# Optimization experiments

Hardware: AMD Instinct MI355X
Metric: run time of the kernel (lower is better)

The kernel has to match this reference:

```python
import jax, jax.numpy as jnp
import numpy as np

H = 400      # LSTM hidden units
K = 10       # attention window mixture components (mixtures=30 -> alpha/beta/kappa of size K)
V = 61       # vocab_size
NOUT = 121   # MDN head: 1 eos + 20*(pi, mu1, mu2, sigma1, sigma2, rho)


def setup_inputs():
    key = jax.random.key(0)
    ks = jax.random.split(key, 12)
    B, T, U = 32, 600, 64
    s = 0.05
    d = {}
    d['strokes'] = jax.random.normal(ks[0], (B, T, 3), jnp.float32)
    d['sentence'] = jax.random.uniform(ks[1], (B, U, V), dtype=jnp.float32)
    d['W1'] = jax.random.normal(ks[2], (3 + V, 4 * H), jnp.float32) * s
    d['U1r'] = jax.random.normal(ks[3], (H, 4 * H), jnp.float32) * s
    d['b1'] = jnp.zeros((4 * H,), jnp.float32)
    d['Ww'] = jax.random.normal(ks[4], (H, 3 * K), jnp.float32) * s
    d['bw'] = jnp.zeros((3 * K,), jnp.float32)
    d['W2'] = jax.random.normal(ks[5], (3 + V + H, 4 * H), jnp.float32) * s
    d['U2r'] = jax.random.normal(ks[6], (H, 4 * H), jnp.float32) * s
    d['b2'] = jnp.zeros((4 * H,), jnp.float32)
    d['W3'] = jax.random.normal(ks[7], (3 + V + H, 4 * H), jnp.float32) * s
    d['U3r'] = jax.random.normal(ks[8], (H, 4 * H), jnp.float32) * s
    d['b3'] = jnp.zeros((4 * H,), jnp.float32)
    d['Wm'] = jax.random.normal(ks[9], (3 * H, NOUT), jnp.float32) * s
    d['bm'] = jnp.zeros((NOUT,), jnp.float32)
    return d


def _lstm(x_tbd, W, Ur, b, h0, c0):
    # standard Keras-order (i, f, g, o) LSTM over time-major input [T,B,D]
    def step(carry, xt):
        h, c = carry
        z = xt @ W + h @ Ur + b
        i, f, g, o = jnp.split(z, 4, axis=-1)
        c = jax.nn.sigmoid(f) * c + jax.nn.sigmoid(i) * jnp.tanh(g)
        h = jax.nn.sigmoid(o) * jnp.tanh(c)
        return (h, c), h
    _, hs = jax.lax.scan(step, (h0, c0), x_tbd)
    return hs


def _forward(strokes, sentence, W1, U1r, b1, Ww, bw, W2, U2r, b2, W3, U3r, b3, Wm, bm):
    B, T, _ = strokes.shape
    U = sentence.shape[1]
    u_grid = jnp.arange(U, dtype=strokes.dtype)           # character positions
    x_tb = jnp.transpose(strokes, (1, 0, 2))               # [T,B,3]
    h0 = jnp.zeros((B, H), strokes.dtype)
    w0 = jnp.zeros((B, V), strokes.dtype)
    k0 = jnp.zeros((B, K), strokes.dtype)

    def step1(carry, xt):
        # Graves synthesis windowed LSTM cell: LSTM on [x_t, w_{t-1}],
        # then Gaussian-mixture soft attention over the sentence.
        h, c, w, kappa = carry
        xin = jnp.concatenate([xt, w], axis=-1)            # [B, 3+V]
        z = xin @ W1 + h @ U1r + b1
        i, f, g, o = jnp.split(z, 4, axis=-1)
        c = jax.nn.sigmoid(f) * c + jax.nn.sigmoid(i) * jnp.tanh(g)
        h = jax.nn.sigmoid(o) * jnp.tanh(c)
        p = h @ Ww + bw                                    # [B, 3K]
        alpha = jnp.exp(p[:, :K])
        beta = jnp.exp(p[:, K:2 * K])
        kappa = kappa + jnp.exp(p[:, 2 * K:])
        # phi(u) = sum_k alpha_k exp(-beta_k (kappa_k - u)^2)  -> [B,U]
        phi = jnp.einsum('bk,bku->bu', alpha,
                         jnp.exp(-beta[:, :, None] * (kappa[:, :, None] - u_grid) ** 2))
        w = jnp.einsum('bu,buv->bv', phi, sentence)        # soft window [B,V]
        return (h, c, w, kappa), jnp.concatenate([h, w], axis=-1)

    _, o1 = jax.lax.scan(step1, (h0, h0, w0, k0), x_tb)    # [T,B,H+V]
    lstm1 = o1[:, :, :H]
    win = o1[:, :, H:]
    in2 = jnp.concatenate([x_tb, win, lstm1], axis=-1)     # skip1: [T,B,3+V+H]
    lstm2 = _lstm(in2, W2, U2r, b2, h0, h0)
    in3 = jnp.concatenate([x_tb, win, lstm2], axis=-1)     # skip2
    lstm3 = _lstm(in3, W3, U3r, b3, h0, h0)
    y = jnp.concatenate([lstm1, lstm2, lstm3], axis=-1) @ Wm + bm  # [T,B,121]
    # MDN mixture coefficients
    e = jax.nn.sigmoid(y[..., 0:1])
    pi = jax.nn.softmax(y[..., 1:21], axis=-1)
    mu1 = y[..., 21:41]
    mu2 = y[..., 41:61]
    s1 = jnp.exp(y[..., 61:81])
    s2 = jnp.exp(y[..., 81:101])
    rho = jnp.tanh(y[..., 101:121])
    out = jnp.concatenate([e, pi, mu1, mu2, s1, s2, rho], axis=-1)
    return jnp.transpose(out, (1, 0, 2))                   # [B,T,121]


def reference(strokes, sentence, W1, U1r, b1, Ww, bw, W2, U2r, b2, W3, U3r, b3, Wm, bm):
    return _forward(strokes, sentence, W1, U1r, b1, Ww, bw, W2, U2r, b2, W3, U3r, b3, Wm, bm)
```

## Files before the change

kernel.cpp:

```cpp
#include <hip/hip_runtime.h>
#include <math.h>

#define T 600
#define NBLK 235

#define FL1 256
#define FL2 768
#define FL3 1280
#define FLB 1792
#define SH1 2304
#define SH2 2880
#define SH3 3520

#define OFF_UT1 8192
#define SZ_UT1 (1600*480)
#define OFF_UT2 (OFF_UT1 + SZ_UT1)
#define SZ_UT2 (1600*960)
#define OFF_UT3 (OFF_UT2 + SZ_UT2)
#define OFF_WWT (OFF_UT3 + SZ_UT2)
#define SZ_WWT (30*400)
#define OFF_H1 (OFF_WWT + SZ_WWT)
#define SZ_H (600*32*400)
#define OFF_H2 (OFF_H1 + SZ_H)
#define OFF_H3 (OFF_H2 + SZ_H)
#define OFF_W  (OFF_H3 + SZ_H)
#define SZ_W (600*32*61)

#define LDS_W    0
#define LDS_V    19280
#define LDS_Z    34640
#define LDS_C    35408
#define LDS_TOT  35600

__device__ __forceinline__ float sigm(float x) { return 1.f/(1.f+expf(-x)); }

#define WBAR() do { \
    asm volatile("s_waitcnt lgkmcnt(0)" ::: "memory"); \
    __builtin_amdgcn_sched_barrier(0); \
} while (0)

__global__ void init_ws(unsigned* uws) {
    for (int i = threadIdx.x + blockIdx.x*blockDim.x; i < 8192; i += blockDim.x*gridDim.x)
        uws[i] = 0u;
}

__global__ void build_ut(float* __restrict__ ws,
                         const float* __restrict__ W1, const float* __restrict__ U1r,
                         const float* __restrict__ W2, const float* __restrict__ U2r,
                         const float* __restrict__ W3, const float* __restrict__ U3r,
                         const float* __restrict__ Ww) {
    const long N1 = 1600L*480, N2 = 1600L*960;
    const long total = N1 + 2*N2 + 30L*400;
    for (long i = blockIdx.x*(long)blockDim.x + threadIdx.x; i < total;
         i += (long)gridDim.x*blockDim.x) {
        if (i < N1) {
            long c = i / 480, k = i % 480;
            float v = 0.f;
            if (k < 64) v = W1[k*1600 + c];
            else if (k < 464) v = U1r[(k-64)*1600 + c];
            ws[OFF_UT1 + c*480 + k] = v;
        } else if (i < N1 + N2) {
            long ii = i - N1; long c = ii/960, k = ii%960;
            float v = 0.f;
            if (k < 464) v = W2[k*1600 + c];
            else if (k >= 480 && k < 880) v = U2r[(k-480)*1600 + c];
            ws[OFF_UT2 + c*960 + k] = v;
        } else if (i < N1 + 2*N2) {
            long ii = i - N1 - N2; long c = ii/960, k = ii%960;
            float v = 0.f;
            if (k < 464) v = W3[k*1600 + c];
            else if (k >= 480 && k < 880) v = U3r[(k-480)*1600 + c];
            ws[OFF_UT3 + c*960 + k] = v;
        } else {
            long ii = i - N1 - 2*N2; long n = ii/400, k = ii%400;
            ws[OFF_WWT + n*400 + k] = Ww[k*30 + n];
        }
    }
}

__device__ __forceinline__ unsigned ld_cohere(const unsigned* p) {
    unsigned v;
    asm volatile("global_load_dword %0, %1, off sc0 sc1\n\t"
                 "s_waitcnt vmcnt(0)"
                 : "=v"(v) : "v"(p) : "memory");
    return v;
}
__device__ __forceinline__ void st_wt(float* p, float v) {
    asm volatile("global_store_dword %0, %1, off sc0 sc1\n\t"
                 "s_waitcnt vmcnt(0)"
                 :: "v"(p), "v"(v) : "memory");
}
__device__ __forceinline__ void publish(unsigned* flags, unsigned v) {
    #pragma unroll
    for (int r = 0; r < 8; ++r)
        asm volatile("global_store_dword %0, %1, off sc0 sc1"
                     :: "v"(flags + r*64), "v"(v) : "memory");
    asm volatile("s_waitcnt vmcnt(0)" ::: "memory");
}
__device__ __forceinline__ void wait_flag(const unsigned* p, unsigned tgt) {
    int it = 0;
    while (ld_cohere(p) < tgt) {
        if (it > 64) __builtin_amdgcn_s_sleep(2);
        ++it;
    }
}
__device__ __forceinline__ void arrive2(unsigned* shard, unsigned gsize,
                                        unsigned* master, unsigned n,
                                        unsigned* flags, unsigned ep1) {
    unsigned old = __hip_atomic_fetch_add(shard, 1u, __ATOMIC_RELAXED,
                                          __HIP_MEMORY_SCOPE_AGENT);
    if (old + 1u == gsize * ep1) {
        unsigned o2 = __hip_atomic_fetch_add(master, gsize, __ATOMIC_RELAXED,
                                             __HIP_MEMORY_SCOPE_AGENT);
        if (o2 + gsize == n * ep1) publish(flags, ep1);
    }
}
__device__ __forceinline__ void arrive1(unsigned* master, unsigned n,
                                        unsigned* flags, unsigned ep1) {
    unsigned old = __hip_atomic_fetch_add(master, 1u, __ATOMIC_RELAXED,
                                          __HIP_MEMORY_SCOPE_AGENT);
    if (old + 1u == n * ep1) publish(flags, ep1);
}

template<int NQ, int KCN, int K4S, int LO, int HI>
__device__ __forceinline__ void gemm_pass(const float4* __restrict__ w4,
                                          const float4* __restrict__ v4,
                                          int lc0, int kc, int bq, int kofs4,
                                          float acc[8][4]) {
    #pragma unroll
    for (int q = 0; q < NQ; ++q) {
        int kfv = q*KCN + kc;
        if (kfv >= LO && kfv < HI) {
            int xv = kfv ^ ((kfv >> 3) & 7);
            int kfw = kofs4 + kfv;
            int xw = kfw ^ ((kfw >> 3) & 7);
            float4 va[8];
            #pragma unroll
            for (int i = 0; i < 8; ++i) va[i] = v4[(bq*8+i)*120 + xv];
            #pragma unroll
            for (int j = 0; j < 4; ++j) {
                float4 u = w4[(lc0+j)*K4S + xw];
                #pragma unroll
                for (int i = 0; i < 8; ++i)
                    acc[i][j] += va[i].x*u.x + va[i].y*u.y + va[i].z*u.z + va[i].w*u.w;
            }
        }
    }
}

__launch_bounds__(512)
__global__ void hw_main(float* __restrict__ ws,
                        const float* __restrict__ strokes, const float* __restrict__ sentence,
                        const float* __restrict__ b1, const float* __restrict__ b2,
                        const float* __restrict__ b3, const float* __restrict__ bw) {
    extern __shared__ float S[];
    const int tid = threadIdx.x;
    const int bid = blockIdx.x;
    unsigned* uws = (unsigned*)ws;
    unsigned* root1 = uws + 0;
    unsigned* root2 = uws + 64;
    unsigned* root3 = uws + 128;
    unsigned* rootB = uws + 192;
    const int rep = (bid & 7) * 64;
    const unsigned* fl1r = uws + FL1 + rep;
    const unsigned* fl2r = uws + FL2 + rep;
    const unsigned* flBr = uws + FLB + rep;

    int role, unit0 = 0, nu = 0, L = 0, b0a = 0;
    const float* utp = nullptr; const float* biasp = nullptr; float* hout = nullptr;
    if (bid < 67)       { role = 0; L = bid;      unit0 = L*6; nu = (bid==66)?4:6; utp = ws+OFF_UT1; biasp = b1; hout = ws+OFF_H1; }
    else if (bid < 147) { role = 1; L = bid-67;   unit0 = L*5; nu = 5;             utp = ws+OFF_UT2; biasp = b2; hout = ws+OFF_H2; }
    else if (bid < 227) { role = 2; L = bid-147;  unit0 = L*5; nu = 5;             utp = ws+OFF_UT3; biasp = b3; hout = ws+OFF_H3; }
    else                { role = 3; b0a = (bid-227)*4; }

    if (role <= 2) {
        const int NC = 4*nu;
        const int KCN = (role == 0) ? 20 : 24;
        const int K4S = (role == 0) ? 121 : 241;
        const int K4TOT = (role == 0) ? 120 : 240;
        const int uts = (role == 0) ? 480 : 960;
        float4* w4 = (float4*)S;
        float4* v4 = (float4*)(S + LDS_V);
        float*  vf = S + LDS_V;
        float*  z_lds = S + LDS_Z;
        float*  c_lds = S + LDS_C;

        for (int idx = tid; idx < NC*K4TOT; idx += 512) {
            int colL = idx / K4TOT, kf = idx % K4TOT;
            int gcol = (colL/nu)*400 + unit0 + (colL%nu);
            float4 val = *(const float4*)(utp + (size_t)gcol*uts + kf*4);
            w4[colL*K4S + (kf ^ ((kf>>3)&7))] = val;
        }
        for (int i = tid; i < 192; i += 512) c_lds[i] = 0.f;

        const int tile = tid / KCN, kc = tid % KCN;
        const int bq = tile / nu, cq = tile % nu;
        const bool act = (tile < 4*nu);
        float bias0 = 0.f, bias1 = 0.f;
        if (tid < 32*NC)       { int lc = tid % NC;        bias0 = biasp[(lc/nu)*400 + unit0 + (lc%nu)]; }
        if (tid + 512 < 32*NC) { int lc = (tid+512) % NC;  bias1 = biasp[(lc/nu)*400 + unit0 + (lc%nu)]; }
        const unsigned nrole = (role == 0) ? 67u : 80u;
        unsigned* mymaster = (role == 0) ? root1 : ((role == 1) ? root2 : root3);
        unsigned* myfl     = uws + ((role == 0) ? FL1 : ((role == 1) ? FL2 : FL3));
        const unsigned* myflr = uws + ((role == 0) ? FL1 : ((role == 1) ? FL2 : FL3)) + rep;
        unsigned* myshard;
        {
            int shbase = (role == 0) ? SH1 : ((role == 1) ? SH2 : SH3);
            myshard = uws + shbase + (L >> 3) * 64;
        }
        const unsigned gsize = (unsigned)(((int)nrole - (L >> 3)*8 < 8) ? ((int)nrole - (L >> 3)*8) : 8);
        __syncthreads();

        for (int t = 0; t < T; ++t) {
            float acc[8][4];
            #pragma unroll
            for (int i = 0; i < 8; ++i)
                #pragma unroll
                for (int j = 0; j < 4; ++j) acc[i][j] = 0.f;

            if (role == 0) {
                if (tid == 0 && t > 0) wait_flag(myflr, (unsigned)t);
                __syncthreads();
                const float* hsrc = (t > 0) ? (ws + OFF_H1 + (size_t)(t-1)*12800) : nullptr;
                for (int idx = tid; idx < 32*104; idx += 512) {
                    int b = idx/104, kf = 16 + idx%104;
                    float4 val = {0.f,0.f,0.f,0.f};
                    if (kf < 116 && hsrc) val = *(const float4*)(hsrc + b*400 + (kf*4 - 64));
                    v4[b*120 + (kf ^ ((kf>>3)&7))] = val;
                }
                __syncthreads();
                if (act) gemm_pass<6,20,121,16,116>(w4, v4, cq*4, kc, bq, 0, acc);
                if (tid == 0 && t > 0) wait_flag(flBr, (unsigned)t);
                __syncthreads();
                const float* wsrc = (t > 0) ? (ws + OFF_W + (size_t)(t-1)*1952) : nullptr;
                {
                    int b = tid / 16, kf = tid % 16;
                    if (b < 32) {
                        float4 val;
                        if (kf == 0) {
                            const float* xp = strokes + ((size_t)b*600 + t)*3;
                            val.x = xp[0]; val.y = xp[1]; val.z = xp[2];
                            val.w = wsrc ? wsrc[b*61] : 0.f;
                        } else {
                            int k0 = kf*4 - 3;
                            if (wsrc) { val.x = wsrc[b*61+k0]; val.y = wsrc[b*61+k0+1];
                                        val.z = wsrc[b*61+k0+2]; val.w = wsrc[b*61+k0+3]; }
                            else { val.x=val.y=val.z=val.w=0.f; }
                        }
                        v4[b*120 + (kf ^ ((kf>>3)&7))] = val;
                    }
                }
                __syncthreads();
                if (act) gemm_pass<6,20,121,0,16>(w4, v4, cq*4, kc, bq, 0, acc);
            } else {
                if (tid == 0) wait_flag((role==1) ? fl1r : fl2r, (unsigned)(t+1));
                __syncthreads();
                const float* hsrc = ws + ((role==1)?OFF_H1:OFF_H2) + (size_t)t*12800;
                for (int idx = tid; idx < 32*104; idx += 512) {
                    int b = idx/104, kf = 16 + idx%104;
                    float4 val = {0.f,0.f,0.f,0.f};
                    if (kf < 116) val = *(const float4*)(hsrc + b*400 + (kf*4 - 64));
                    v4[b*120 + (kf ^ ((kf>>3)&7))] = val;
                }
                __syncthreads();
                if (act) gemm_pass<5,24,241,16,116>(w4, v4, cq*4, kc, bq, 0, acc);
                if (tid == 0) wait_flag(flBr, (unsigned)(t+1));
                __syncthreads();
                const float* wsrc = ws + OFF_W + (size_t)t*1952;
                {
                    int b = tid / 16, kf = tid % 16;
                    if (b < 32) {
                        float4 val;
                        if (kf == 0) {
                            const float* xp = strokes + ((size_t)b*600 + t)*3;
                            val.x = xp[0]; val.y = xp[1]; val.z = xp[2];
                            val.w = wsrc[b*61];
                        } else {
                            int k0 = kf*4 - 3;
                            val.x = wsrc[b*61+k0]; val.y = wsrc[b*61+k0+1];
                            val.z = wsrc[b*61+k0+2]; val.w = wsrc[b*61+k0+3];
                        }
                        v4[b*120 + (kf ^ ((kf>>3)&7))] = val;
                    }
                }
                __syncthreads();
                if (act) gemm_pass<5,24,241,0,16>(w4, v4, cq*4, kc, bq, 0, acc);
                __syncthreads();
                if (tid == 0 && t > 0) wait_flag(myflr, (unsigned)t);
                __syncthreads();
                const float* hp2 = (t > 0) ? (ws + ((role==1)?OFF_H2:OFF_H3) + (size_t)(t-1)*12800) : nullptr;
                for (int idx = tid; idx < 32*120; idx += 512) {
                    int b = idx/120, kf = idx%120;
                    float4 val = {0.f,0.f,0.f,0.f};
                    if (kf < 100 && hp2) val = *(const float4*)(hp2 + b*400 + kf*4);
                    v4[b*120 + (kf ^ ((kf>>3)&7))] = val;
                }
                __syncthreads();
                if (act) gemm_pass<5,24,241,0,100>(w4, v4, cq*4, kc, bq, 120, acc);
            }

            __syncthreads();
            const int halfk = (KCN+1)/2;
            const int SCRW = NC*32 + 4;
            const int NO = 32*NC;
            if (act && kc < halfk) {
                #pragma unroll
                for (int i = 0; i < 8; ++i) {
                    float4 w;
                    w.x=acc[i][0]; w.y=acc[i][1]; w.z=acc[i][2]; w.w=acc[i][3];
                    *(float4*)&vf[kc*SCRW + (bq*8+i)*NC + cq*4] = w;
                }
            }
            __syncthreads();
            float zs0 = 0.f, zs1 = 0.f;
            if (tid < NO)       for (int k2 = 0; k2 < halfk; ++k2) zs0 += vf[k2*SCRW + tid];
            if (tid + 512 < NO) for (int k2 = 0; k2 < halfk; ++k2) zs1 += vf[k2*SCRW + tid + 512];
            __syncthreads();
            if (act && kc >= halfk) {
                #pragma unroll
                for (int i = 0; i < 8; ++i) {
                    float4 w;
                    w.x=acc[i][0]; w.y=acc[i][1]; w.z=acc[i][2]; w.w=acc[i][3];
                    *(float4*)&vf[(kc-halfk)*SCRW + (bq*8+i)*NC + cq*4] = w;
                }
            }
            __syncthreads();
            const int rem = KCN - halfk;
            if (tid < NO) {
                for (int k2 = 0; k2 < rem; ++k2) zs0 += vf[k2*SCRW + tid];
                z_lds[tid] = zs0 + bias0;
            }
            if (tid + 512 < NO) {
                for (int k2 = 0; k2 < rem; ++k2) zs1 += vf[k2*SCRW + tid + 512];
                z_lds[tid + 512] = zs1 + bias1;
            }
            __syncthreads();
            if (tid < 32*nu) {
                int b = tid & 31, ju = tid >> 5;
                float zi = z_lds[b*NC + ju];
                float zf = z_lds[b*NC + nu + ju];
                float zg = z_lds[b*NC + 2*nu + ju];
                float zo = z_lds[b*NC + 3*nu + ju];
                float cP = c_lds[b*6 + ju];
                float cN = sigm(zf)*cP + sigm(zi)*tanhf(zg);
                float hN = sigm(zo)*tanhf(cN);
                c_lds[b*6 + ju] = cN;
                st_wt(&hout[(size_t)t*12800 + b*400 + unit0 + ju], hN);
            }
            __syncthreads();
            if (tid == 0) arrive2(myshard, gsize, mymaster, nrole, myfl, (unsigned)(t+1));
        }
    } else {
        const int wv = tid >> 6, lane = tid & 63;
        float* hb   = S;
        float* pb   = S + 1600 + (tid>>6)*32;
        float* ab   = S + 1792 + (tid>>6)*32;
        float* kap  = S + 1984 + (tid>>6)*16;
        float* phiW = S + 2112 + (tid>>6)*64;
        float* sentl= S + 2368;
        float* wwt  = S + 2368 + 15616;
        float* hbW  = hb + wv*400;
        float4* hb4 = (float4*)hbW;

        for (int i = tid; i < 64; i += 512) (S + 1984)[i] = 0.f;
        for (int i = tid; i < 15616; i += 512) sentl[i] = sentence[(size_t)b0a*3904 + i];
        for (int i = tid; i < 12000; i += 512) {
            int n = i/400, k = i%400;
            wwt[n*404 + k] = ws[OFF_WWT + i];
        }
        float bwv = (lane < 60 && !(lane & 1)) ? bw[lane >> 1] : 0.f;
        __syncthreads();

        for (int t = 0; t < T; ++t) {
            if (wv < 4) {
                {
                    int it = 0;
                    while (ld_cohere(fl1r) < (unsigned)(t+1)) {
                        if (it > 64) __builtin_amdgcn_s_sleep(2);
                        ++it;
                    }
                }
                const float* h1t = ws + OFF_H1 + (size_t)t*12800 + (size_t)(b0a+wv)*400;
                for (int i = lane; i < 100; i += 64)
                    hb4[i] = *(const float4*)(h1t + i*4);
                WBAR();
                if (lane < 60) {
                    int n = lane >> 1, hf = lane & 1;
                    const float4* ww4 = (const float4*)(wwt + n*404) + hf*50;
                    const float4* hh4 = hb4 + hf*50;
                    float a = 0.f;
                    #pragma unroll 5
                    for (int i = 0; i < 50; ++i) {
                        float4 h = hh4[i], w = ww4[i];
                        a += h.x*w.x + h.y*w.y + h.z*w.z + h.w*w.w;
                    }
                    a += __shfl_xor(a, 1);
                    if (hf == 0) pb[n] = a + bwv;
                }
                WBAR();
                if (lane < 10) {
                    ab[lane]      = expf(pb[lane]);
                    ab[16 + lane] = expf(pb[10 + lane]);
                    kap[lane]    += expf(pb[20 + lane]);
                }
                WBAR();
                {
                    float uf = (float)lane, ph = 0.f;
                    #pragma unroll
                    for (int k0 = 0; k0 < 10; ++k0) {
                        float d = kap[k0] - uf;
                        ph += ab[k0]*expf(-ab[16 + k0]*d*d);
                    }
                    phiW[lane] = ph;
                }
                WBAR();
                if (lane < 61) {
                    const float* sp = sentl + wv*3904 + lane;
                    float wvv = 0.f;
                    #pragma unroll 4
                    for (int u = 0; u < 64; ++u) wvv += phiW[u]*sp[u*61];
                    st_wt(&ws[OFF_W + (size_t)t*1952 + (size_t)(b0a+wv)*61 + lane], wvv);
                }
            }
            __syncthreads();
            if (tid == 0) arrive1(rootB, 8u, uws + FLB, (unsigned)(t+1));
        }
    }
}

__launch_bounds__(256)
__global__ void out_proj(const float* __restrict__ ws, const float* __restrict__ Wm,
                         const float* __restrict__ bm, float* __restrict__ out) {
    __shared__ __align__(16) float hc[8*1200];
    __shared__ float yy[8*121];
    __shared__ float sm2[16];
    const int tid = threadIdx.x;
    const long rowbase = (long)blockIdx.x * 8;
    const float* h1h = ws + OFF_H1;
    const float* h2h = ws + OFF_H2;
    const float* h3h = ws + OFF_H3;
    for (int idx = tid; idx < 8*1200; idx += 256) {
        int i = idx/1200, k = idx%1200;
        long r = rowbase + i; int t = (int)(r >> 5), b = (int)(r & 31);
        float v;
        if (k < 400)      v = h1h[(size_t)t*12800 + b*400 + k];
        else if (k < 800) v = h2h[(size_t)t*12800 + b*400 + (k-400)];
        else              v = h3h[(size_t)t*12800 + b*400 + (k-800)];
        hc[i*1200 + k] = v;
    }
    __syncthreads();
    const int j = tid & 127, rr = tid >> 7;
    if (j < 121) {
        float a0=0.f, a1=0.f, a2=0.f, a3=0.f;
        const float* r0 = &hc[(rr*4+0)*1200];
        const float* r1 = &hc[(rr*4+1)*1200];
        const float* r2 = &hc[(rr*4+2)*1200];
        const float* r3 = &hc[(rr*4+3)*1200];
        for (int k = 0; k < 1200; ++k) {
            float wm = Wm[(size_t)k*121 + j];
            a0 += r0[k]*wm; a1 += r1[k]*wm; a2 += r2[k]*wm; a3 += r3[k]*wm;
        }
        float bb = bm[j];
        yy[(rr*4+0)*121 + j] = a0 + bb;
        yy[(rr*4+1)*121 + j] = a1 + bb;
        yy[(rr*4+2)*121 + j] = a2 + bb;
        yy[(rr*4+3)*121 + j] = a3 + bb;
    }
    __syncthreads();
    if (tid < 8) {
        const float* yr = &yy[tid*121];
        float m = yr[1];
        for (int q = 2; q < 21; ++q) m = fmaxf(m, yr[q]);
        float ssum = 0.f;
        for (int q = 1; q < 21; ++q) ssum += expf(yr[q] - m);
        sm2[tid*2] = m; sm2[tid*2+1] = ssum;
    }
    __syncthreads();
    if (j < 121) {
        for (int i2 = 0; i2 < 4; ++i2) {
            int i = rr*4 + i2;
            long r = rowbase + i; int t = (int)(r >> 5), b = (int)(r & 31);
            float y = yy[i*121 + j], o;
            if (j == 0)      o = 1.f/(1.f + expf(-y));
            else if (j < 21) o = expf(y - sm2[i*2]) / sm2[i*2+1];
            else if (j < 61) o = y;
            else if (j < 101) o = expf(y);
            else             o = tanhf(y);
            out[((size_t)b*600 + t)*121 + j] = o;
        }
    }
}

extern "C" void kernel_launch(void* const* d_in, const int* in_sizes, int n_in,
                              void* d_out, int out_size, void* d_ws, size_t ws_size,
                              hipStream_t stream) {
    const float* strokes  = (const float*)d_in[0];
    const float* sentence = (const float*)d_in[1];
    const float* W1  = (const float*)d_in[2];
    const float* U1r = (const float*)d_in[3];
    const float* b1  = (const float*)d_in[4];
    const float* Ww  = (const float*)d_in[5];
    const float* bw  = (const float*)d_in[6];
    const float* W2  = (const float*)d_in[7];
    const float* U2r = (const float*)d_in[8];
    const float* b2  = (const float*)d_in[9];
    const float* W3  = (const float*)d_in[10];
    const float* U3r = (const float*)d_in[11];
    const float* b3  = (const float*)d_in[12];
    const float* Wm  = (const float*)d_in[13];
    const float* bm  = (const float*)d_in[14];
    float* ws = (float*)d_ws;
    float* out = (float*)d_out;

    const int dyn_bytes = LDS_TOT * 4;
    (void)hipFuncSetAttribute((const void*)hw_main,
                              hipFuncAttributeMaxDynamicSharedMemorySize, dyn_bytes);

    init_ws<<<dim3(4), dim3(512), 0, stream>>>((unsigned*)ws);
    build_ut<<<dim3(1024), dim3(256), 0, stream>>>(ws, W1, U1r, W2, U2r, W3, U3r, Ww);
    hw_main<<<dim3(NBLK), dim3(512), dyn_bytes, stream>>>(ws, strokes, sentence, b1, b2, b3, bw);
    out_proj<<<dim3(2400), dim3(256), 0, stream>>>(ws, Wm, bm, out);
}
```

Measured before the change: 10.35 ms.

## Replace atomic-counter grid barriers with per-block sentinel words polled by waiters

Drops the hierarchical atomic fetch-add arrival scheme (shard counters, master counter, replicated publish flags). Each block now writes its step number to its own padded sentinel word, and waiters use one wavefront to poll all producer sentinels and take the minimum. This removes atomic contention and the serial arrive-then-publish chain from every timestep's critical path. The cost is that each wait reads 67 or 80 words instead of one flag, which adds polling traffic.

```diff
diff --git a/kernel.cpp b/kernel.cpp
--- a/kernel.cpp
+++ b/kernel.cpp
@@ -4,13 +4,10 @@
 #define T 600
 #define NBLK 235
 
-#define FL1 256
-#define FL2 768
-#define FL3 1280
-#define FLB 1792
-#define SH1 2304
-#define SH2 2880
-#define SH3 3520
+#define SEN1 256
+#define SEN2 1536
+#define SEN3 3072
+#define SENB 4608
 
 #define OFF_UT1 8192
 #define SZ_UT1 (1600*480)
@@ -90,36 +87,25 @@
                  "s_waitcnt vmcnt(0)"
                  :: "v"(p), "v"(v) : "memory");
 }
-__device__ __forceinline__ void publish(unsigned* flags, unsigned v) {
-    #pragma unroll
-    for (int r = 0; r < 8; ++r)
-        asm volatile("global_store_dword %0, %1, off sc0 sc1"
-                     :: "v"(flags + r*64), "v"(v) : "memory");
-    asm volatile("s_waitcnt vmcnt(0)" ::: "memory");
-}
-__device__ __forceinline__ void wait_flag(const unsigned* p, unsigned tgt) {
-    int it = 0;
-    while (ld_cohere(p) < tgt) {
-        if (it > 64) __builtin_amdgcn_s_sleep(2);
-        ++it;
-    }
-}
-__device__ __forceinline__ void arrive2(unsigned* shard, unsigned gsize,
-                                        unsigned* master, unsigned n,
-                                        unsigned* flags, unsigned ep1) {
-    unsigned old = __hip_atomic_fetch_add(shard, 1u, __ATOMIC_RELAXED,
-                                          __HIP_MEMORY_SCOPE_AGENT);
-    if (old + 1u == gsize * ep1) {
-        unsigned o2 = __hip_atomic_fetch_add(master, gsize, __ATOMIC_RELAXED,
-                                             __HIP_MEMORY_SCOPE_AGENT);
-        if (o2 + gsize == n * ep1) publish(flags, ep1);
-    }
-}
-__device__ __forceinline__ void arrive1(unsigned* master, unsigned n,
-                                        unsigned* flags, unsigned ep1) {
-    unsigned old = __hip_atomic_fetch_add(master, 1u, __ATOMIC_RELAXED,
-                                          __HIP_MEMORY_SCOPE_AGENT);
-    if (old + 1u == n * ep1) publish(flags, ep1);
+__device__ __forceinline__ void st_wt_u(unsigned* p, unsigned v) {
+    asm volatile("global_store_dword %0, %1, off sc0 sc1\n\t"
+                 "s_waitcnt vmcnt(0)"
+                 :: "v"(p), "v"(v) : "memory");
+}
+__device__ __forceinline__ void wait_sen(const unsigned* sen, int count,
+                                         unsigned tgt, int tid) {
+    if (tid < 64) {
+        for (;;) {
+            unsigned m = 0xFFFFFFFFu;
+            for (int i = tid; i < count; i += 64) {
+                unsigned v = ld_cohere(sen + (size_t)i*16);
+                m = (v < m) ? v : m;
+            }
+            if (__all(m >= tgt)) break;
+            __builtin_amdgcn_s_sleep(1);
+        }
+    }
+    __syncthreads();
 }
 
 template<int NQ, int KCN, int K4S, int LO, int HI>
@@ -157,21 +143,17 @@
     const int tid = threadIdx.x;
     const int bid = blockIdx.x;
     unsigned* uws = (unsigned*)ws;
-    unsigned* root1 = uws + 0;
-    unsigned* root2 = uws + 64;
-    unsigned* root3 = uws + 128;
-    unsigned* rootB = uws + 192;
-    const int rep = (bid & 7) * 64;
-    const unsigned* fl1r = uws + FL1 + rep;
-    const unsigned* fl2r = uws + FL2 + rep;
-    const unsigned* flBr = uws + FLB + rep;
+    const unsigned* sen1 = uws + SEN1;
+    const unsigned* sen2 = uws + SEN2;
+    const unsigned* sen3 = uws + SEN3;
+    const unsigned* senB = uws + SENB;
 
     int role, unit0 = 0, nu = 0, L = 0, b0a = 0;
     const float* utp = nullptr; const float* biasp = nullptr; float* hout = nullptr;
     if (bid < 67)       { role = 0; L = bid;      unit0 = L*6; nu = (bid==66)?4:6; utp = ws+OFF_UT1; biasp = b1; hout = ws+OFF_H1; }
     else if (bid < 147) { role = 1; L = bid-67;   unit0 = L*5; nu = 5;             utp = ws+OFF_UT2; biasp = b2; hout = ws+OFF_H2; }
     else if (bid < 227) { role = 2; L = bid-147;  unit0 = L*5; nu = 5;             utp = ws+OFF_UT3; biasp = b3; hout = ws+OFF_H3; }
-    else                { role = 3; b0a = (bid-227)*4; }
+    else                { role = 3; L = bid-227;  b0a = L*4; }
 
     if (role <= 2) {
         const int NC = 4*nu;
@@ -199,16 +181,9 @@
         float bias0 = 0.f, bias1 = 0.f;
         if (tid < 32*NC)       { int lc = tid % NC;        bias0 = biasp[(lc/nu)*400 + unit0 + (lc%nu)]; }
         if (tid + 512 < 32*NC) { int lc = (tid+512) % NC;  bias1 = biasp[(lc/nu)*400 + unit0 + (lc%nu)]; }
-        const unsigned nrole = (role == 0) ? 67u : 80u;
-        unsigned* mymaster = (role == 0) ? root1 : ((role == 1) ? root2 : root3);
-        unsigned* myfl     = uws + ((role == 0) ? FL1 : ((role == 1) ? FL2 : FL3));
-        const unsigned* myflr = uws + ((role == 0) ? FL1 : ((role == 1) ? FL2 : FL3)) + rep;
-        unsigned* myshard;
-        {
-            int shbase = (role == 0) ? SH1 : ((role == 1) ? SH2 : SH3);
-            myshard = uws + shbase + (L >> 3) * 64;
-        }
-        const unsigned gsize = (unsigned)(((int)nrole - (L >> 3)*8 < 8) ? ((int)nrole - (L >> 3)*8) : 8);
+        const int nrole = (role == 0) ? 67 : 80;
+        const unsigned* mysen = (role == 0) ? sen1 : ((role == 1) ? sen2 : sen3);
+        unsigned* myword = (unsigned*)mysen + (size_t)L*16;
         __syncthreads();
 
         for (int t = 0; t < T; ++t) {
@@ -219,8 +194,7 @@
                 for (int j = 0; j < 4; ++j) acc[i][j] = 0.f;
 
             if (role == 0) {
-                if (tid == 0 && t > 0) wait_flag(myflr, (unsigned)t);
-                __syncthreads();
+                if (t > 0) wait_sen(sen1, 67, (unsigned)t, tid);
                 const float* hsrc = (t > 0) ? (ws + OFF_H1 + (size_t)(t-1)*12800) : nullptr;
                 for (int idx = tid; idx < 32*104; idx += 512) {
                     int b = idx/104, kf = 16 + idx%104;
@@ -230,8 +204,7 @@
                 }
                 __syncthreads();
                 if (act) gemm_pass<6,20,121,16,116>(w4, v4, cq*4, kc, bq, 0, acc);
-                if (tid == 0 && t > 0) wait_flag(flBr, (unsigned)t);
-                __syncthreads();
+                if (t > 0) wait_sen(senB, 8, (unsigned)t, tid);
                 const float* wsrc = (t > 0) ? (ws + OFF_W + (size_t)(t-1)*1952) : nullptr;
                 {
                     int b = tid / 16, kf = tid % 16;
@@ -253,8 +226,8 @@
                 __syncthreads();
                 if (act) gemm_pass<6,20,121,0,16>(w4, v4, cq*4, kc, bq, 0, acc);
             } else {
-                if (tid == 0) wait_flag((role==1) ? fl1r : fl2r, (unsigned)(t+1));
-                __syncthreads();
+                if (role == 1) wait_sen(sen1, 67, (unsigned)(t+1), tid);
+                else           wait_sen(sen2, 80, (unsigned)(t+1), tid);
                 const float* hsrc = ws + ((role==1)?OFF_H1:OFF_H2) + (size_t)t*12800;
                 for (int idx = tid; idx < 32*104; idx += 512) {
                     int b = idx/104, kf = 16 + idx%104;
@@ -264,8 +237,7 @@
                 }
                 __syncthreads();
                 if (act) gemm_pass<5,24,241,16,116>(w4, v4, cq*4, kc, bq, 0, acc);
-                if (tid == 0) wait_flag(flBr, (unsigned)(t+1));
-                __syncthreads();
+                wait_sen(senB, 8, (unsigned)(t+1), tid);
                 const float* wsrc = ws + OFF_W + (size_t)t*1952;
                 {
                     int b = tid / 16, kf = tid % 16;
@@ -286,8 +258,7 @@
                 __syncthreads();
                 if (act) gemm_pass<5,24,241,0,16>(w4, v4, cq*4, kc, bq, 0, acc);
                 __syncthreads();
-                if (tid == 0 && t > 0) wait_flag(myflr, (unsigned)t);
-                __syncthreads();
+                if (t > 0) wait_sen(mysen, nrole, (unsigned)t, tid);
                 const float* hp2 = (t > 0) ? (ws + ((role==1)?OFF_H2:OFF_H3) + (size_t)(t-1)*12800) : nullptr;
                 for (int idx = tid; idx < 32*120; idx += 512) {
                     int b = idx/120, kf = idx%120;
@@ -348,7 +319,7 @@
                 st_wt(&hout[(size_t)t*12800 + b*400 + unit0 + ju], hN);
             }
             __syncthreads();
-            if (tid == 0) arrive2(myshard, gsize, mymaster, nrole, myfl, (unsigned)(t+1));
+            if (tid == 0) st_wt_u(myword, (unsigned)(t+1));
         }
     } else {
         const int wv = tid >> 6, lane = tid & 63;
@@ -361,6 +332,7 @@
         float* wwt  = S + 2368 + 15616;
         float* hbW  = hb + wv*400;
         float4* hb4 = (float4*)hbW;
+        unsigned* myword = (unsigned*)senB + (size_t)L*16;
 
         for (int i = tid; i < 64; i += 512) (S + 1984)[i] = 0.f;
         for (int i = tid; i < 15616; i += 512) sentl[i] = sentence[(size_t)b0a*3904 + i];
@@ -372,14 +344,8 @@
         __syncthreads();
 
         for (int t = 0; t < T; ++t) {
+            wait_sen(sen1, 67, (unsigned)(t+1), tid);
             if (wv < 4) {
-                {
-                    int it = 0;
-                    while (ld_cohere(fl1r) < (unsigned)(t+1)) {
-                        if (it > 64) __builtin_amdgcn_s_sleep(2);
-                        ++it;
-                    }
-                }
                 const float* h1t = ws + OFF_H1 + (size_t)t*12800 + (size_t)(b0a+wv)*400;
                 for (int i = lane; i < 100; i += 64)
                     hb4[i] = *(const float4*)(h1t + i*4);
@@ -423,7 +389,7 @@
                 }
             }
             __syncthreads();
-            if (tid == 0) arrive1(rootB, 8u, uws + FLB, (unsigned)(t+1));
+            if (tid == 0) st_wt_u(myword, (unsigned)(t+1));
         }
     }
 }
```

Result: no change. 10.43 ms (+0.8%).
